# Performance work log

Measured on AMD Instinct MI355X. Metric: run time of the kernel, lower is better.

The kernel has to match this reference:

```python
import jax, jax.numpy as jnp
import numpy as np

BN_EPS = 1e-3  # Keras BatchNormalization default epsilon


def setup_inputs() -> dict:
    key = jax.random.key(0)
    ks = jax.random.split(key, 16)
    B, N, M = 4, 16384, 4096
    C1, C2 = 128, 256
    mlp = [256, 128]
    cin = C2 + C1
    inp = {
        "xyz1": jax.random.normal(ks[0], (B, N, 3), dtype=jnp.float32),
        "xyz2": jax.random.normal(ks[1], (B, M, 3), dtype=jnp.float32),
        "points1": jax.random.normal(ks[2], (B, N, C1), dtype=jnp.float32),
        "points2": jax.random.normal(ks[3], (B, M, C2), dtype=jnp.float32),
    }
    k = 4
    for i, cout in enumerate(mlp):
        inp[f"w{i}"] = jax.random.normal(ks[k], (cin, cout), dtype=jnp.float32) * (1.0 / np.sqrt(cin)); k += 1
        inp[f"g{i}"] = jnp.ones((cout,), dtype=jnp.float32) + 0.1 * jax.random.normal(ks[k], (cout,), dtype=jnp.float32); k += 1
        inp[f"b{i}"] = 0.1 * jax.random.normal(ks[k], (cout,), dtype=jnp.float32); k += 1
        inp[f"m{i}"] = 0.1 * jax.random.normal(ks[k], (cout,), dtype=jnp.float32); k += 1
        inp[f"v{i}"] = 0.5 + jax.random.uniform(ks[k], (cout,), dtype=jnp.float32); k += 1
        cin = cout
    return inp


def _three_nn(xyz1, xyz2):
    # squared pairwise distances [B,N,M] via ||a||^2 + ||b||^2 - 2ab
    n1 = jnp.sum(xyz1 * xyz1, axis=-1)                      # [B,N]
    n2 = jnp.sum(xyz2 * xyz2, axis=-1)                      # [B,M]
    d2 = n1[:, :, None] + n2[:, None, :] - 2.0 * jnp.einsum("bnc,bmc->bnm", xyz1, xyz2)
    d2 = jnp.maximum(d2, 0.0)
    neg, idx = jax.lax.top_k(-d2, 3)                        # 3 smallest distances
    return -neg, idx                                        # dist [B,N,3], idx [B,N,3]


def reference(xyz1, xyz2, points1, points2,
              w0, g0, b0, m0, v0, w1, g1, b1, m1, v1):
    dist, idx = _three_nn(xyz1, xyz2)
    dist = jnp.maximum(dist, 1e-10)
    inv = 1.0 / dist                                        # [B,N,3]
    weight = inv / jnp.sum(inv, axis=2, keepdims=True)      # [B,N,3]
    # three_interpolate: irregular gather + weighted sum
    gathered = jax.vmap(lambda p, i: p[i])(points2, idx)    # [B,N,3,C2]
    interp = jnp.einsum("bnk,bnkc->bnc", weight, gathered)  # [B,N,C2]
    x = jnp.concatenate([interp, points1], axis=2)          # [B,N,C2+C1]
    # 1x1 Conv2D (no bias) + BN(inference) + ReLU stack
    for w, g, b, m, v in ((w0, g0, b0, m0, v0), (w1, g1, b1, m1, v1)):
        x = jnp.einsum("bnc,cd->bnd", x, w)
        x = (x - m) * (g * jax.lax.rsqrt(v + BN_EPS)) + b
        x = jax.nn.relu(x)
    return x
```

## Files before the change

kernel.cpp:

```cpp
#include <hip/hip_runtime.h>
#include <hip/hip_bf16.h>

typedef __bf16 bf16x8 __attribute__((ext_vector_type(8)));
typedef float  f32x4  __attribute__((ext_vector_type(4)));
typedef unsigned short ushort_t;
typedef unsigned int   uint_t;

__device__ __forceinline__ ushort_t f2bf(float f) {
    union { float f; uint_t u; } v; v.f = f;
    uint_t r = v.u + 0x7fffu + ((v.u >> 16) & 1u);
    return (ushort_t)(r >> 16);
}

__device__ __forceinline__ void async_copy16(const void* g, void* l) {
    __builtin_amdgcn_global_load_lds(
        (const __attribute__((address_space(1))) unsigned int*)g,
        (__attribute__((address_space(3))) unsigned int*)l, 16, 0, 0);
}

#define BATCH 4
#define NPTS  16384
#define MPTS  4096
#define C1    128
#define C2    256
#define NCHUNK 8
#define CHUNK  (MPTS / NCHUNK)

__global__ __launch_bounds__(256) void prep_kernel(
    const float* __restrict__ w0, const float* __restrict__ w1,
    const float* __restrict__ g0, const float* __restrict__ b0,
    const float* __restrict__ m0, const float* __restrict__ v0,
    const float* __restrict__ g1, const float* __restrict__ b1,
    const float* __restrict__ m1, const float* __restrict__ v1,
    ushort_t* __restrict__ wt0, ushort_t* __restrict__ wt1,
    float* __restrict__ sc0, float* __restrict__ sh0,
    float* __restrict__ sc1, float* __restrict__ sh1) {
    int i = blockIdx.x * 256 + threadIdx.x;
    if (i < 256 * 384) {
        int n = i / 384, k = i % 384;
        wt0[i] = f2bf(w0[k * 256 + n]);
    }
    if (i < 128 * 256) {
        int n = i / 256, k = i % 256;
        wt1[i] = f2bf(w1[k * 128 + n]);
    }
    if (i < 256) { float s = g0[i] * rsqrtf(v0[i] + 1e-3f); sc0[i] = s; sh0[i] = b0[i] - m0[i] * s; }
    if (i < 128) { float s = g1[i] * rsqrtf(v1[i] + 1e-3f); sc1[i] = s; sh1[i] = b1[i] - m1[i] * s; }
}

__global__ __launch_bounds__(256) void knn_partial(
    const float* __restrict__ xyz1, const float* __restrict__ xyz2,
    float* __restrict__ pd, int* __restrict__ pi) {
    __shared__ __align__(16) float s[3 * CHUNK];
    float* sx = s;
    float* sy = s + CHUNK;
    float* sz = s + 2 * CHUNK;
    const int t  = threadIdx.x;
    const int qb = blockIdx.x;
    const int c  = blockIdx.y;
    const int b  = blockIdx.z;
#pragma unroll
    for (int j = 0; j < CHUNK / 256; j++) {
        const int m = j * 256 + t;
        const float* g = xyz2 + ((long)b * MPTS + c * CHUNK + m) * 3;
        sx[m] = g[0]; sy[m] = g[1]; sz[m] = g[2];
    }
    __syncthreads();
    const int n = qb * 256 + t;
    const long base = ((long)b * NPTS + n) * 3;
    const float qx = xyz1[base], qy = xyz1[base + 1], qz = xyz1[base + 2];
    float d0 = 3.4e38f, d1 = 3.4e38f, d2 = 3.4e38f;
    int   i0 = 0, i1 = 0, i2 = 0;
    const int mbase = c * CHUNK;
    for (int g = 0; g < CHUNK; g += 4) {
        const float4 X = *(const float4*)&sx[g];
        const float4 Y = *(const float4*)&sy[g];
        const float4 Z = *(const float4*)&sz[g];
        const float xs[4] = {X.x, X.y, X.z, X.w};
        const float ys[4] = {Y.x, Y.y, Y.z, Y.w};
        const float zs[4] = {Z.x, Z.y, Z.z, Z.w};
#pragma unroll
        for (int j = 0; j < 4; j++) {
            const float dx = qx - xs[j], dy = qy - ys[j], dz = qz - zs[j];
            const float d = dx * dx + dy * dy + dz * dz;
            const int m = mbase + g + j;
            const bool c0 = d < d0, c1 = d < d1, c2 = d < d2;
            const float nd2 = c1 ? d1 : (c2 ? d : d2);
            const int   ni2 = c1 ? i1 : (c2 ? m : i2);
            const float nd1 = c0 ? d0 : (c1 ? d : d1);
            const int   ni1 = c0 ? i0 : (c1 ? m : i1);
            d0 = c0 ? d : d0;  i0 = c0 ? m : i0;
            d1 = nd1; i1 = ni1; d2 = nd2; i2 = ni2;
        }
    }
    const long ng = (long)b * NPTS + n;
    const long po = ((long)c * (BATCH * NPTS) + ng) * 3;
    pd[po] = d0; pd[po + 1] = d1; pd[po + 2] = d2;
    pi[po] = i0; pi[po + 1] = i1; pi[po + 2] = i2;
}

__global__ __launch_bounds__(256) void knn_merge(
    const float* __restrict__ pd, const int* __restrict__ pi,
    int* __restrict__ idx, float* __restrict__ wgt) {
    const long n = blockIdx.x * 256 + threadIdx.x;
    float d0 = 3.4e38f, d1 = 3.4e38f, d2 = 3.4e38f;
    int   i0 = 0, i1 = 0, i2 = 0;
#pragma unroll
    for (int c = 0; c < NCHUNK; c++) {
        const long po = ((long)c * (BATCH * NPTS) + n) * 3;
#pragma unroll
        for (int k = 0; k < 3; k++) {
            const float d = pd[po + k];
            const int   m = pi[po + k];
            const bool c0 = d < d0, c1 = d < d1, c2 = d < d2;
            const float nd2 = c1 ? d1 : (c2 ? d : d2);
            const int   ni2 = c1 ? i1 : (c2 ? m : i2);
            const float nd1 = c0 ? d0 : (c1 ? d : d1);
            const int   ni1 = c0 ? i0 : (c1 ? m : i1);
            d0 = c0 ? d : d0;  i0 = c0 ? m : i0;
            d1 = nd1; i1 = ni1; d2 = nd2; i2 = ni2;
        }
    }
    d0 = fmaxf(d0, 1e-10f); d1 = fmaxf(d1, 1e-10f); d2 = fmaxf(d2, 1e-10f);
    const float w0 = 1.f / d0, w1 = 1.f / d1, w2 = 1.f / d2;
    const float rs = 1.f / (w0 + w1 + w2);
    const long o = n * 3;
    idx[o] = i0; idx[o + 1] = i1; idx[o + 2] = i2;
    wgt[o] = w0 * rs; wgt[o + 1] = w1 * rs; wgt[o + 2] = w2 * rs;
}

__global__ __launch_bounds__(256) void interp_kernel(
    const float* __restrict__ points1, const float* __restrict__ points2,
    const int* __restrict__ idx, const float* __restrict__ wgt,
    ushort_t* __restrict__ x0) {
    const int wave = (blockIdx.x * 256 + threadIdx.x) >> 6;
    const int lane = threadIdx.x & 63;
    const int b = wave >> 14;
    const int n = wave & 16383;
    const long o = (long)wave * 3;
    int i0 = idx[o], i1 = idx[o + 1], i2 = idx[o + 2];
    i0 = min(max(i0, 0), MPTS - 1);
    i1 = min(max(i1, 0), MPTS - 1);
    i2 = min(max(i2, 0), MPTS - 1);
    const float w0 = wgt[o], w1 = wgt[o + 1], w2 = wgt[o + 2];
    const float4* p0 = (const float4*)(points2 + ((long)b * MPTS + i0) * C2);
    const float4* p1 = (const float4*)(points2 + ((long)b * MPTS + i1) * C2);
    const float4* p2 = (const float4*)(points2 + ((long)b * MPTS + i2) * C2);
    float4 a = p0[lane], bb = p1[lane], c = p2[lane];
    ushort4 u;
    u.x = f2bf(w0 * a.x + w1 * bb.x + w2 * c.x);
    u.y = f2bf(w0 * a.y + w1 * bb.y + w2 * c.y);
    u.z = f2bf(w0 * a.z + w1 * bb.z + w2 * c.z);
    u.w = f2bf(w0 * a.w + w1 * bb.w + w2 * c.w);
    ((ushort4*)(x0 + (long)wave * 384))[lane] = u;
    const float2* q = (const float2*)(points1 + ((long)b * NPTS + n) * C1);
    float2 t = q[lane];
    uint_t packed = (uint_t)f2bf(t.x) | ((uint_t)f2bf(t.y) << 16);
    ((uint_t*)(x0 + (long)wave * 384 + 256))[lane] = packed;
}

template <int K, bool OUT_BF16>
__global__ __launch_bounds__(256) void gemm_bn_relu(
    const ushort_t* __restrict__ A,
    const ushort_t* __restrict__ Bt,
    const float* __restrict__ scale, const float* __restrict__ shift,
    void* __restrict__ outp, int ldout) {
    __shared__ ushort_t lds[8192];
    ushort_t* ldsA = lds;
    ushort_t* ldsB = lds + 4096;
    const int tid  = threadIdx.x;
    const int wv   = tid >> 6;
    const int lane = tid & 63;
    const int q    = lane >> 4, l16 = lane & 15;
    const int rowBase = blockIdx.x * 128;
    const int colBase = blockIdx.y * 128;
    const int wrow = (wv & 1) * 64, wcol = (wv >> 1) * 64;
    f32x4 acc[4][4] = {};

    for (int kk = 0; kk < K; kk += 32) {
#pragma unroll
        for (int ch = 0; ch < 2; ch++) {
            const int linear = ch * 4096 + tid * 16;
            const int row = linear >> 6;
            const int brow = linear & 63;
            const char* ga = (const char*)A + ((long)(rowBase + row) * K + kk) * 2 + brow;
            async_copy16(ga, (char*)ldsA + ch * 4096 + wv * 1024);
            const char* gb = (const char*)Bt + ((long)(colBase + row) * K + kk) * 2 + brow;
            async_copy16(gb, (char*)ldsB + ch * 4096 + wv * 1024);
        }
        __syncthreads();
        bf16x8 af[4], bfr[4];
#pragma unroll
        for (int t = 0; t < 4; t++) {
            const int r = wrow + t * 16 + l16;
            af[t]  = *(const bf16x8*)((const char*)ldsA + r * 64 + q * 16);
            const int c = wcol + t * 16 + l16;
            bfr[t] = *(const bf16x8*)((const char*)ldsB + c * 64 + q * 16);
        }
#pragma unroll
        for (int tr = 0; tr < 4; tr++)
#pragma unroll
            for (int tc = 0; tc < 4; tc++)
                acc[tr][tc] = __builtin_amdgcn_mfma_f32_16x16x32_bf16(af[tr], bfr[tc], acc[tr][tc], 0, 0, 0);
        __syncthreads();
    }
#pragma unroll
    for (int tc = 0; tc < 4; tc++) {
        const int col = colBase + wcol + tc * 16 + l16;
        const float sc = scale[col], sh = shift[col];
#pragma unroll
        for (int tr = 0; tr < 4; tr++) {
            const int row0 = rowBase + wrow + tr * 16 + q * 4;
#pragma unroll
            for (int r = 0; r < 4; r++) {
                float v = acc[tr][tc][r];
                v = fmaxf(v * sc + sh, 0.0f);
                const long off = (long)(row0 + r) * ldout + col;
                if (OUT_BF16) ((ushort_t*)outp)[off] = f2bf(v);
                else          ((float*)outp)[off]    = v;
            }
        }
    }
}

extern "C" void kernel_launch(void* const* d_in, const int* in_sizes, int n_in,
                              void* d_out, int out_size, void* d_ws, size_t ws_size,
                              hipStream_t stream) {
    const float* xyz1    = (const float*)d_in[0];
    const float* xyz2    = (const float*)d_in[1];
    const float* points1 = (const float*)d_in[2];
    const float* points2 = (const float*)d_in[3];
    const float* w0 = (const float*)d_in[4];
    const float* g0 = (const float*)d_in[5];
    const float* b0 = (const float*)d_in[6];
    const float* m0 = (const float*)d_in[7];
    const float* v0 = (const float*)d_in[8];
    const float* w1 = (const float*)d_in[9];
    const float* g1 = (const float*)d_in[10];
    const float* b1 = (const float*)d_in[11];
    const float* m1 = (const float*)d_in[12];
    const float* v1 = (const float*)d_in[13];

    char* ws = (char*)d_ws;
    int*      idx = (int*)ws;
    float*    wgt = (float*)(ws + 786432);
    ushort_t* wt0 = (ushort_t*)(ws + 1572864);
    ushort_t* wt1 = (ushort_t*)(ws + 1769472);
    float*    sc0 = (float*)(ws + 1835008);
    float*    sh0 = sc0 + 256;
    float*    sc1 = sh0 + 256;
    float*    sh1 = sc1 + 128;
    ushort_t* x0  = (ushort_t*)(ws + 2097152);
    ushort_t* y1  = (ushort_t*)(ws + 2097152 + 50331648);
    float* pd = (float*)(ws + 2097152);
    int*   pi = (int*)(ws + 2097152 + 6291456);

    prep_kernel<<<384, 256, 0, stream>>>(w0, w1, g0, b0, m0, v0, g1, b1, m1, v1,
                                         wt0, wt1, sc0, sh0, sc1, sh1);
    knn_partial<<<dim3(NPTS / 256, NCHUNK, BATCH), 256, 0, stream>>>(xyz1, xyz2, pd, pi);
    knn_merge<<<(BATCH * NPTS) / 256, 256, 0, stream>>>(pd, pi, idx, wgt);
    interp_kernel<<<(BATCH * NPTS) / 4, 256, 0, stream>>>(points1, points2, idx, wgt, x0);
    gemm_bn_relu<384, true ><<<dim3((BATCH * NPTS) / 128, 2), 256, 0, stream>>>(
        x0, wt0, sc0, sh0, (void*)y1, 256);
    gemm_bn_relu<256, false><<<dim3((BATCH * NPTS) / 128, 1), 256, 0, stream>>>(
        y1, wt1, sc1, sh1, d_out, 128);
}
```

Measured before the change: 312.0 us.

## Process two queries per thread in knn_partial and read candidates directly from global

Each thread now handles two query points, so every candidate coordinate loaded is reused across both, and the grid is halved. The shared-memory staging and its barrier are removed. Candidate xyz values are read straight from global memory as three float4 loads per group of four points, which are wave-uniform and likely go through the scalar or L1 cache. In exchange there are fewer blocks and more registers per thread, and the candidate loads depend on cache behaviour instead of LDS.

```diff
diff --git a/kernel.cpp b/kernel.cpp
--- a/kernel.cpp
+++ b/kernel.cpp
@@ -51,52 +51,63 @@
 __global__ __launch_bounds__(256) void knn_partial(
     const float* __restrict__ xyz1, const float* __restrict__ xyz2,
     float* __restrict__ pd, int* __restrict__ pi) {
-    __shared__ __align__(16) float s[3 * CHUNK];
-    float* sx = s;
-    float* sy = s + CHUNK;
-    float* sz = s + 2 * CHUNK;
     const int t  = threadIdx.x;
     const int qb = blockIdx.x;
     const int c  = blockIdx.y;
     const int b  = blockIdx.z;
-#pragma unroll
-    for (int j = 0; j < CHUNK / 256; j++) {
-        const int m = j * 256 + t;
-        const float* g = xyz2 + ((long)b * MPTS + c * CHUNK + m) * 3;
-        sx[m] = g[0]; sy[m] = g[1]; sz[m] = g[2];
-    }
-    __syncthreads();
-    const int n = qb * 256 + t;
-    const long base = ((long)b * NPTS + n) * 3;
-    const float qx = xyz1[base], qy = xyz1[base + 1], qz = xyz1[base + 2];
-    float d0 = 3.4e38f, d1 = 3.4e38f, d2 = 3.4e38f;
-    int   i0 = 0, i1 = 0, i2 = 0;
-    const int mbase = c * CHUNK;
+    const int n0 = qb * 512 + t;
+    const int n1 = n0 + 256;
+    const long baseA = ((long)b * NPTS + n0) * 3;
+    const long baseB = ((long)b * NPTS + n1) * 3;
+    const float qxa = xyz1[baseA], qya = xyz1[baseA + 1], qza = xyz1[baseA + 2];
+    const float qxb = xyz1[baseB], qyb = xyz1[baseB + 1], qzb = xyz1[baseB + 2];
+
+    float d0a = 3.4e38f, d1a = 3.4e38f, d2a = 3.4e38f;
+    int   i0a = 0, i1a = 0, i2a = 0;
+    float d0b = 3.4e38f, d1b = 3.4e38f, d2b = 3.4e38f;
+    int   i0b = 0, i1b = 0, i2b = 0;
+
+    auto ins = [](float d, int m, float& D0, int& I0, float& D1, int& I1,
+                  float& D2, int& I2) {
+        const bool c0 = d < D0, c1 = d < D1, c2 = d < D2;
+        const float nd2 = c1 ? D1 : (c2 ? d : D2);
+        const int   ni2 = c1 ? I1 : (c2 ? m : I2);
+        const float nd1 = c0 ? D0 : (c1 ? d : D1);
+        const int   ni1 = c0 ? I0 : (c1 ? m : I1);
+        D0 = c0 ? d : D0; I0 = c0 ? m : I0;
+        D1 = nd1; I1 = ni1; D2 = nd2; I2 = ni2;
+    };
+
+    const int mb = c * CHUNK;
+    const float* __restrict__ gp = xyz2 + ((long)b * MPTS + mb) * 3;
     for (int g = 0; g < CHUNK; g += 4) {
-        const float4 X = *(const float4*)&sx[g];
-        const float4 Y = *(const float4*)&sy[g];
-        const float4 Z = *(const float4*)&sz[g];
-        const float xs[4] = {X.x, X.y, X.z, X.w};
-        const float ys[4] = {Y.x, Y.y, Y.z, Y.w};
-        const float zs[4] = {Z.x, Z.y, Z.z, Z.w};
+        const float4 P0 = *(const float4*)(gp + 3 * g);
+        const float4 P1 = *(const float4*)(gp + 3 * g + 4);
+        const float4 P2 = *(const float4*)(gp + 3 * g + 8);
+        const float px[4] = {P0.x, P0.w, P1.z, P2.y};
+        const float py[4] = {P0.y, P1.x, P1.w, P2.z};
+        const float pz[4] = {P0.z, P1.y, P2.x, P2.w};
 #pragma unroll
         for (int j = 0; j < 4; j++) {
-            const float dx = qx - xs[j], dy = qy - ys[j], dz = qz - zs[j];
-            const float d = dx * dx + dy * dy + dz * dz;
-            const int m = mbase + g + j;
-            const bool c0 = d < d0, c1 = d < d1, c2 = d < d2;
-            const float nd2 = c1 ? d1 : (c2 ? d : d2);
-            const int   ni2 = c1 ? i1 : (c2 ? m : i2);
-            const float nd1 = c0 ? d0 : (c1 ? d : d1);
-            const int   ni1 = c0 ? i0 : (c1 ? m : i1);
-            d0 = c0 ? d : d0;  i0 = c0 ? m : i0;
-            d1 = nd1; i1 = ni1; d2 = nd2; i2 = ni2;
-        }
-    }
-    const long ng = (long)b * NPTS + n;
-    const long po = ((long)c * (BATCH * NPTS) + ng) * 3;
-    pd[po] = d0; pd[po + 1] = d1; pd[po + 2] = d2;
-    pi[po] = i0; pi[po + 1] = i1; pi[po + 2] = i2;
+            const int m = mb + g + j;
+            {
+                const float dx = px[j] - qxa, dy = py[j] - qya, dz = pz[j] - qza;
+                const float d = dx * dx + dy * dy + dz * dz;
+                ins(d, m, d0a, i0a, d1a, i1a, d2a, i2a);
+            }
+            {
+                const float dx = px[j] - qxb, dy = py[j] - qyb, dz = pz[j] - qzb;
+                const float d = dx * dx + dy * dy + dz * dz;
+                ins(d, m, d0b, i0b, d1b, i1b, d2b, i2b);
+            }
+        }
+    }
+    const long poA = ((long)c * (BATCH * NPTS) + (long)b * NPTS + n0) * 3;
+    const long poB = ((long)c * (BATCH * NPTS) + (long)b * NPTS + n1) * 3;
+    pd[poA] = d0a; pd[poA + 1] = d1a; pd[poA + 2] = d2a;
+    pi[poA] = i0a; pi[poA + 1] = i1a; pi[poA + 2] = i2a;
+    pd[poB] = d0b; pd[poB + 1] = d1b; pd[poB + 2] = d2b;
+    pi[poB] = i0b; pi[poB + 1] = i1b; pi[poB + 2] = i2b;
 }
 
 __global__ __launch_bounds__(256) void knn_merge(
@@ -257,7 +268,7 @@
 
     prep_kernel<<<384, 256, 0, stream>>>(w0, w1, g0, b0, m0, v0, g1, b1, m1, v1,
                                          wt0, wt1, sc0, sh0, sc1, sh1);
-    knn_partial<<<dim3(NPTS / 256, NCHUNK, BATCH), 256, 0, stream>>>(xyz1, xyz2, pd, pi);
+    knn_partial<<<dim3(NPTS / 512, NCHUNK, BATCH), 256, 0, stream>>>(xyz1, xyz2, pd, pi);
     knn_merge<<<(BATCH * NPTS) / 256, 256, 0, stream>>>(pd, pi, idx, wgt);
     interp_kernel<<<(BATCH * NPTS) / 4, 256, 0, stream>>>(points1, points2, idx, wgt, x0);
     gemm_bn_relu<384, true ><<<dim3((BATCH * NPTS) / 128, 2), 256, 0, stream>>>(
```

Result: slower. 324.4 us (+4.0%).

## Use norm-expansion distances with wave-uniform skip in KNN and fewer chunks

Applied to the files above, without the earlier changes.

The KNN partial kernel now computes a reduced distance |b|^2 - 2a·b with three FMAs, using per-point squared norms precomputed in shared memory. The query norm is added back in the merge kernel. The top-3 insertion is skipped whenever no lane in the wave has a candidate better than its current third-best. The chunk count drops from 8 to 4, so each block scans a longer candidate list and merges are cheaper, at the cost of fewer blocks for parallelism and slightly different floating-point rounding.

```diff
diff --git a/kernel.cpp b/kernel.cpp
--- a/kernel.cpp
+++ b/kernel.cpp
@@ -23,7 +23,7 @@
 #define MPTS  4096
 #define C1    128
 #define C2    256
-#define NCHUNK 8
+#define NCHUNK 4
 #define CHUNK  (MPTS / NCHUNK)
 
 __global__ __launch_bounds__(256) void prep_kernel(
@@ -51,10 +51,7 @@
 __global__ __launch_bounds__(256) void knn_partial(
     const float* __restrict__ xyz1, const float* __restrict__ xyz2,
     float* __restrict__ pd, int* __restrict__ pi) {
-    __shared__ __align__(16) float s[3 * CHUNK];
-    float* sx = s;
-    float* sy = s + CHUNK;
-    float* sz = s + 2 * CHUNK;
+    __shared__ __align__(16) float sx[CHUNK], sy[CHUNK], sz[CHUNK], sw[CHUNK];
     const int t  = threadIdx.x;
     const int qb = blockIdx.x;
     const int c  = blockIdx.y;
@@ -63,43 +60,48 @@
     for (int j = 0; j < CHUNK / 256; j++) {
         const int m = j * 256 + t;
         const float* g = xyz2 + ((long)b * MPTS + c * CHUNK + m) * 3;
-        sx[m] = g[0]; sy[m] = g[1]; sz[m] = g[2];
+        const float x = g[0], y = g[1], z = g[2];
+        sx[m] = x; sy[m] = y; sz[m] = z; sw[m] = x * x + y * y + z * z;
     }
     __syncthreads();
     const int n = qb * 256 + t;
     const long base = ((long)b * NPTS + n) * 3;
     const float qx = xyz1[base], qy = xyz1[base + 1], qz = xyz1[base + 2];
+    const float nx = -2.f * qx, ny = -2.f * qy, nz = -2.f * qz;
     float d0 = 3.4e38f, d1 = 3.4e38f, d2 = 3.4e38f;
     int   i0 = 0, i1 = 0, i2 = 0;
-    const int mbase = c * CHUNK;
+    const int mb = c * CHUNK;
     for (int g = 0; g < CHUNK; g += 4) {
         const float4 X = *(const float4*)&sx[g];
         const float4 Y = *(const float4*)&sy[g];
         const float4 Z = *(const float4*)&sz[g];
+        const float4 W = *(const float4*)&sw[g];
         const float xs[4] = {X.x, X.y, X.z, X.w};
         const float ys[4] = {Y.x, Y.y, Y.z, Y.w};
         const float zs[4] = {Z.x, Z.y, Z.z, Z.w};
+        const float ws[4] = {W.x, W.y, W.z, W.w};
 #pragma unroll
         for (int j = 0; j < 4; j++) {
-            const float dx = qx - xs[j], dy = qy - ys[j], dz = qz - zs[j];
-            const float d = dx * dx + dy * dy + dz * dz;
-            const int m = mbase + g + j;
-            const bool c0 = d < d0, c1 = d < d1, c2 = d < d2;
-            const float nd2 = c1 ? d1 : (c2 ? d : d2);
-            const int   ni2 = c1 ? i1 : (c2 ? m : i2);
-            const float nd1 = c0 ? d0 : (c1 ? d : d1);
-            const int   ni1 = c0 ? i0 : (c1 ? m : i1);
-            d0 = c0 ? d : d0;  i0 = c0 ? m : i0;
-            d1 = nd1; i1 = ni1; d2 = nd2; i2 = ni2;
-        }
-    }
-    const long ng = (long)b * NPTS + n;
-    const long po = ((long)c * (BATCH * NPTS) + ng) * 3;
+            const float s = fmaf(xs[j], nx, fmaf(ys[j], ny, fmaf(zs[j], nz, ws[j])));
+            if (__ballot(s < d2)) {
+                const int m = mb + g + j;
+                const bool c0 = s < d0, c1 = s < d1, c2 = s < d2;
+                const float nd2 = c1 ? d1 : (c2 ? s : d2);
+                const int   ni2 = c1 ? i1 : (c2 ? m : i2);
+                const float nd1 = c0 ? d0 : (c1 ? s : d1);
+                const int   ni1 = c0 ? i0 : (c1 ? m : i1);
+                d0 = c0 ? s : d0; i0 = c0 ? m : i0;
+                d1 = nd1; i1 = ni1; d2 = nd2; i2 = ni2;
+            }
+        }
+    }
+    const long po = ((long)c * (BATCH * NPTS) + (long)b * NPTS + n) * 3;
     pd[po] = d0; pd[po + 1] = d1; pd[po + 2] = d2;
     pi[po] = i0; pi[po + 1] = i1; pi[po + 2] = i2;
 }
 
 __global__ __launch_bounds__(256) void knn_merge(
+    const float* __restrict__ xyz1,
     const float* __restrict__ pd, const int* __restrict__ pi,
     int* __restrict__ idx, float* __restrict__ wgt) {
     const long n = blockIdx.x * 256 + threadIdx.x;
@@ -121,7 +123,11 @@
             d1 = nd1; i1 = ni1; d2 = nd2; i2 = ni2;
         }
     }
-    d0 = fmaxf(d0, 1e-10f); d1 = fmaxf(d1, 1e-10f); d2 = fmaxf(d2, 1e-10f);
+    const float qx = xyz1[n * 3], qy = xyz1[n * 3 + 1], qz = xyz1[n * 3 + 2];
+    const float qn = qx * qx + qy * qy + qz * qz;
+    d0 = fmaxf(d0 + qn, 1e-10f);
+    d1 = fmaxf(d1 + qn, 1e-10f);
+    d2 = fmaxf(d2 + qn, 1e-10f);
     const float w0 = 1.f / d0, w1 = 1.f / d1, w2 = 1.f / d2;
     const float rs = 1.f / (w0 + w1 + w2);
     const long o = n * 3;
@@ -258,7 +264,7 @@
     prep_kernel<<<384, 256, 0, stream>>>(w0, w1, g0, b0, m0, v0, g1, b1, m1, v1,
                                          wt0, wt1, sc0, sh0, sc1, sh1);
     knn_partial<<<dim3(NPTS / 256, NCHUNK, BATCH), 256, 0, stream>>>(xyz1, xyz2, pd, pi);
-    knn_merge<<<(BATCH * NPTS) / 256, 256, 0, stream>>>(pd, pi, idx, wgt);
+    knn_merge<<<(BATCH * NPTS) / 256, 256, 0, stream>>>(xyz1, pd, pi, idx, wgt);
     interp_kernel<<<(BATCH * NPTS) / 4, 256, 0, stream>>>(points1, points2, idx, wgt, x0);
     gemm_bn_relu<384, true ><<<dim3((BATCH * NPTS) / 128, 2), 256, 0, stream>>>(
         x0, wt0, sc0, sh0, (void*)y1, 256);
```

Result: faster. 262.9 us (-15.7%).
